# Optimization experiments

Hardware: AMD Instinct MI355X
Metric: run time of the kernel (lower is better)

## Reference

```python
import jax, jax.numpy as jnp
import numpy as np

N_NODES = 50000
N_EDGES = 800000


def gcn_layer(x, edge_index, W, b):
    """PyG-style GCNConv: add self-loops, symmetric deg^-1/2 normalization,
    linear transform, scatter-sum aggregation at target nodes, plus bias."""
    n = x.shape[0]
    loops = jnp.arange(n)
    src = jnp.concatenate([edge_index[0], loops])  # [E+N]
    dst = jnp.concatenate([edge_index[1], loops])  # [E+N]
    deg = jax.ops.segment_sum(jnp.ones(src.shape, dtype=x.dtype), dst, num_segments=n)
    dinv = jnp.where(deg > 0, jax.lax.rsqrt(deg), jnp.zeros((), x.dtype))
    norm = dinv[src] * dinv[dst]               # [E+N]
    h = x @ W                                   # [N, out]
    msg = norm[:, None] * h[src]                # [E+N, out] gather
    out = jax.ops.segment_sum(msg, dst, num_segments=n)  # scatter-add
    return out + b


def setup_inputs() -> dict:
    key = jax.random.key(0)
    ks = jax.random.split(key, 8)
    features = jax.random.normal(ks[0], (N_NODES, 64), dtype=jnp.float32)
    edge_index1 = jax.random.randint(ks[1], (2, N_EDGES), 0, N_NODES)
    edge_index3 = jax.random.randint(ks[2], (2, N_EDGES), 0, N_NODES)
    edge_index9 = jax.random.randint(ks[3], (2, N_EDGES), 0, N_NODES)

    def glorot(k, fi, fo):
        lim = float(np.sqrt(6.0 / (fi + fo)))
        return jax.random.uniform(k, (fi, fo), minval=-lim, maxval=lim, dtype=jnp.float32)

    W1 = glorot(ks[4], 64, 64)
    W2 = glorot(ks[5], 64, 32)
    W3 = glorot(ks[6], 32, 16)
    b1 = jnp.zeros((64,), jnp.float32)
    b2 = jnp.zeros((32,), jnp.float32)
    b3 = jnp.zeros((16,), jnp.float32)
    return dict(features=features, edge_index1=edge_index1, edge_index3=edge_index3,
                edge_index9=edge_index9, W1=W1, b1=b1, W2=W2, b2=b2, W3=W3, b3=b3)


def reference(features, edge_index1, edge_index3, edge_index9, W1, b1, W2, b2, W3, b3):
    x = jax.nn.relu(gcn_layer(features, edge_index1, W1, b1))  # hop 1
    x = jax.nn.relu(gcn_layer(x, edge_index3, W2, b2))         # hop 3
    x = jax.nn.relu(gcn_layer(x, edge_index9, W3, b3))         # hop 9
    return x
```

## Files before the change

kernel.cpp:

```cpp
#include <hip/hip_runtime.h>
#include <hip/hip_fp16.h>


#define NB   256
#define NL   3
#define TB   (NB * NL)
#define CAPE 6400
#define CAPE_E (CAPE + 8)
#define CH   8192
#define P1T  512
#define EPT  (CH / P1T)
#define P2T  512

__device__ __forceinline__ void decode_chunk(int g, int nc1, int nc2,
                                             const int* s1, const int* d1, int E1,
                                             const int* s2, const int* d2, int E2,
                                             const int* s3, const int* d3, int E3,
                                             const int** src, const int** dst, int* E, int* l,
                                             int* gout) {
    if (g < nc1)            { *src = s1; *dst = d1; *E = E1; *l = 0; }
    else if (g < nc1 + nc2) { *src = s2; *dst = d2; *E = E2; *l = 1; g -= nc1; }
    else                    { *src = s3; *dst = d3; *E = E3; *l = 2; g -= nc1 + nc2; }
    *gout = g;
}

__device__ __forceinline__ void fma4(float4& a, float s, const float4& w) {
    a.x += s * w.x; a.y += s * w.y; a.z += s * w.z; a.w += s * w.w;
}
__device__ __forceinline__ void add4(float4& a, const float4& v) {
    a.x += v.x; a.y += v.y; a.z += v.z; a.w += v.w;
}
__device__ __forceinline__ float4 ldh4(const __half* h, size_t idx4) {
    uint2 r = ((const uint2*)h)[idx4];
    __half2 a = *reinterpret_cast<__half2*>(&r.x);
    __half2 b = *reinterpret_cast<__half2*>(&r.y);
    float2 fa = __half22float2(a), fb = __half22float2(b);
    return make_float4(fa.x, fa.y, fb.x, fb.y);
}
__device__ __forceinline__ void sth4(__half* h, size_t idx4, float4 v) {
    __half2 a = __floats2half2_rn(v.x, v.y);
    __half2 b = __floats2half2_rn(v.z, v.w);
    uint2 r;
    r.x = *reinterpret_cast<unsigned*>(&a);
    r.y = *reinterpret_cast<unsigned*>(&b);
    ((uint2*)h)[idx4] = r;
}

__global__ void __launch_bounds__(P1T) k1_phase1_gemm1(
        const int* __restrict__ s1, const int* __restrict__ d1, int E1,
        const int* __restrict__ s2, const int* __restrict__ d2, int E2,
        const int* __restrict__ s3, const int* __restrict__ d3, int E3,
        int nc1, int nc2, int W, int nchunks,
        int* __restrict__ gcur, unsigned int* __restrict__ pairBuf,
        const float* __restrict__ x0, const float* __restrict__ W1g,
        __half* __restrict__ h1) {
    __shared__ __align__(16) char smem[45056];
    const int t = threadIdx.x;
    if (blockIdx.x < (unsigned)nchunks) {
        int* hist = (int*)smem;
        int* eofs = hist + NB;
        int* bo   = eofs + NB;
        int* lcur = bo + NB;
        unsigned* stage = (unsigned*)(smem + 4096);
        unsigned char* stageQ = (unsigned char*)(smem + 36864);
        for (int i = t; i < NB; i += P1T) hist[i] = 0;
        __syncthreads();
        const int* src; const int* dst; int E, l, g;
        decode_chunk(blockIdx.x, nc1, nc2, s1, d1, E1, s2, d2, E2, s3, d3, E3,
                     &src, &dst, &E, &l, &g);
        const int e0 = g * CH;
        const int lbase = l * NB;
        unsigned pv[EPT];
        int bn[EPT];
        if (E - e0 >= CH) {
            const int4* s4 = (const int4*)(src + e0);
            const int4* d4 = (const int4*)(dst + e0);
#pragma unroll
            for (int w = 0; w < EPT / 4; ++w) {
                int4 sv = s4[t + w * P1T];
                int4 dv = d4[t + w * P1T];
                int q, i = w * 4;
                q = dv.x / W; bn[i+0] = q; pv[i+0] = ((unsigned)sv.x << 9) | (unsigned)(dv.x - q * W);
                q = dv.y / W; bn[i+1] = q; pv[i+1] = ((unsigned)sv.y << 9) | (unsigned)(dv.y - q * W);
                q = dv.z / W; bn[i+2] = q; pv[i+2] = ((unsigned)sv.z << 9) | (unsigned)(dv.z - q * W);
                q = dv.w / W; bn[i+3] = q; pv[i+3] = ((unsigned)sv.w << 9) | (unsigned)(dv.w - q * W);
            }
        } else {
#pragma unroll
            for (int i = 0; i < EPT; ++i) {
                int e = e0 + t + i * P1T;
                if (e < E) {
                    int s = src[e], d = dst[e];
                    int q = d / W;
                    bn[i] = q;
                    pv[i] = ((unsigned)s << 9) | (unsigned)(d - q * W);
                } else bn[i] = -1;
            }
        }
#pragma unroll
        for (int i = 0; i < EPT; ++i)
            if (bn[i] >= 0) atomicAdd(&hist[bn[i]], 1);
        __syncthreads();
        if (t < NB) eofs[t] = hist[t];
        __syncthreads();
        for (int off = 1; off < NB; off <<= 1) {
            int add = (t < NB && t >= off) ? eofs[t - off] : 0;
            __syncthreads();
            if (t < NB) eofs[t] += add;
            __syncthreads();
        }
        const int total = eofs[NB - 1];
        int excl = 0;
        if (t < NB) excl = eofs[t] - hist[t];
        __syncthreads();
        if (t < NB) {
            eofs[t] = excl;
            lcur[t] = excl;
            int c = hist[t];
            bo[t] = (lbase + t) * CAPE + (c ? atomicAdd(&gcur[lbase + t], c) : 0);
        }
        __syncthreads();
#pragma unroll
        for (int i = 0; i < EPT; ++i) {
            if (bn[i] >= 0) {
                int r = atomicAdd(&lcur[bn[i]], 1);
                stage[r] = pv[i];
                stageQ[r] = (unsigned char)bn[i];
            }
        }
        __syncthreads();
        for (int i = t; i < total; i += P1T) {
            int q = stageQ[i];
            int k = bo[q] + (i - eofs[q]);
            if (k < (lbase + q + 1) * CAPE) pairBuf[k] = stage[i];
        }
    } else {
        float* Ws = (float*)smem;
        const int bid = blockIdx.x - nchunks;
        for (int i = t; i < 1024; i += P1T)
            ((float4*)Ws)[i] = ((const float4*)W1g)[i];
        __syncthreads();
        const int tc = t % 16;
        const int tr = t / 16;
        const int row0 = bid * 128 + tr * 4;
        const float4* x4 = (const float4*)x0;
        const float4* Ws4 = (const float4*)Ws;
        float4 acc[4];
#pragma unroll
        for (int r = 0; r < 4; ++r) acc[r] = make_float4(0.f, 0.f, 0.f, 0.f);
        int rowc[4];
#pragma unroll
        for (int r = 0; r < 4; ++r) rowc[r] = min(row0 + r, 49999);
        for (int k0 = 0; k0 < 64; k0 += 4) {
            float4 wv0 = Ws4[(k0 + 0) * 16 + tc];
            float4 wv1 = Ws4[(k0 + 1) * 16 + tc];
            float4 wv2 = Ws4[(k0 + 2) * 16 + tc];
            float4 wv3 = Ws4[(k0 + 3) * 16 + tc];
#pragma unroll
            for (int r = 0; r < 4; ++r) {
                float4 xv = x4[(size_t)rowc[r] * 16 + (k0 / 4)];
                fma4(acc[r], xv.x, wv0);
                fma4(acc[r], xv.y, wv1);
                fma4(acc[r], xv.z, wv2);
                fma4(acc[r], xv.w, wv3);
            }
        }
#pragma unroll
        for (int r = 0; r < 4; ++r) {
            int row = row0 + r;
            if (row < 50000) sth4(h1, (size_t)row * 16 + tc, acc[r]);
        }
    }
}

__global__ void __launch_bounds__(P2T) k2_phase2(
        const unsigned int* __restrict__ pairBuf, const int* __restrict__ gcur,
        int n, int W,
        int* __restrict__ row_ptr, int* __restrict__ cnt_g,
        float* __restrict__ dinv, unsigned short* __restrict__ eidx,
        __half* __restrict__ h1) {
    __shared__ __align__(16) char smem[19456];
    int* lcnt  = (int*)smem;
    int* lscan = lcnt + P2T;
    unsigned short* stage = (unsigned short*)(lscan + P2T);
    float* dloc = (float*)(smem + 17408);
    const int bid = blockIdx.x;
    const int l = bid / NB, k = bid % NB;
    const int lo = k * W;
    const int hi = min(n, lo + W);
    const int Wn = hi - lo;
    const int segE = min(gcur[bid], CAPE);
    const size_t base  = (size_t)bid * CAPE;
    const int    baseE = bid * CAPE_E;
    const int t = threadIdx.x;
    lcnt[t] = 0;
    __syncthreads();
    for (int i = t; i < segE; i += P2T)
        atomicAdd(&lcnt[pairBuf[base + i] & 511u], 1);
    __syncthreads();
    const int v = lcnt[t];
    const int vp = (v + 3) & ~3;
    lscan[t] = vp;
    __syncthreads();
    for (int off = 1; off < P2T; off <<= 1) {
        int add = (t >= off) ? lscan[t - off] : 0;
        __syncthreads();
        lscan[t] += add;
        __syncthreads();
    }
    const int pexcl = lscan[t] - vp;
    const int segEp = lscan[P2T - 1];
    if (t < Wn) {
        int node = l * n + lo + t;
        row_ptr[node] = baseE + pexcl;
        cnt_g[node] = v;
        float dv = rsqrtf((float)v + 1.0f);
        dinv[node] = dv;
        dloc[t] = dv;
    }
    __syncthreads();
    lcnt[t] = pexcl;
    __syncthreads();
    const bool lds_ok = (segEp <= CAPE);
    for (int i = t; i < segE; i += P2T) {
        unsigned p = pairBuf[base + i];
        int pos = atomicAdd(&lcnt[p & 511u], 1);
        unsigned short s = (unsigned short)(p >> 9);
        if (lds_ok) stage[pos] = s;
        else if (pos < CAPE_E) eidx[baseE + pos] = s;
    }
    __syncthreads();
    if (lds_ok) {
        const int4* st4 = (const int4*)stage;
        int4* e4 = (int4*)(eidx + baseE);
        int m16 = (segEp + 7) >> 3;
        for (int i = t; i < m16; i += P2T) e4[i] = st4[i];
    }
    if (l == 0) {
        for (int i = t; i < Wn * 16; i += P2T) {
            int r = i >> 4, c = i & 15;
            size_t idx = (size_t)(lo + r) * 16 + c;
            float4 vv = ldh4(h1, idx);
            float s = dloc[r];
            vv.x *= s; vv.y *= s; vv.z *= s; vv.w *= s;
            sth4(h1, idx, vv);
        }
    }
}

__global__ void __launch_bounds__(256) k3_gather1_gemm2(
        const int* __restrict__ row_ptr, const int* __restrict__ cnt,
        const unsigned short* __restrict__ eidx, const float* __restrict__ dinv1,
        const float* __restrict__ dinv2,
        const __half* __restrict__ h1, const float* __restrict__ b1,
        const float* __restrict__ W2g, __half* __restrict__ h2, int n) {
    __shared__ float xs[16 * 68];
    __shared__ float W2s[64 * 32];
    for (int i = threadIdx.x; i < 512; i += 256)
        ((float4*)W2s)[i] = ((const float4*)W2g)[i];
    const int ln = threadIdx.x >> 4;
    const int f4 = threadIdx.x & 15;
    const int node = blockIdx.x * 16 + ln;
    if (node < n) {
        const int beg = row_ptr[node];
        const int m = cnt[node];
        float4 a0 = make_float4(0.f, 0.f, 0.f, 0.f), a1 = a0, a2 = a0, a3 = a0;
        int j = 0;
        for (; j + 8 <= m; j += 8) {
            ushort4 e0 = *(const ushort4*)(eidx + beg + j);
            ushort4 e1 = *(const ushort4*)(eidx + beg + j + 4);
            add4(a0, ldh4(h1, (size_t)e0.x * 16 + f4));
            add4(a1, ldh4(h1, (size_t)e0.y * 16 + f4));
            add4(a2, ldh4(h1, (size_t)e0.z * 16 + f4));
            add4(a3, ldh4(h1, (size_t)e0.w * 16 + f4));
            add4(a0, ldh4(h1, (size_t)e1.x * 16 + f4));
            add4(a1, ldh4(h1, (size_t)e1.y * 16 + f4));
            add4(a2, ldh4(h1, (size_t)e1.z * 16 + f4));
            add4(a3, ldh4(h1, (size_t)e1.w * 16 + f4));
        }
        if (j + 4 <= m) {
            ushort4 e0 = *(const ushort4*)(eidx + beg + j);
            add4(a0, ldh4(h1, (size_t)e0.x * 16 + f4));
            add4(a1, ldh4(h1, (size_t)e0.y * 16 + f4));
            add4(a2, ldh4(h1, (size_t)e0.z * 16 + f4));
            add4(a3, ldh4(h1, (size_t)e0.w * 16 + f4));
            j += 4;
        }
        for (; j < m; ++j)
            add4(a0, ldh4(h1, (size_t)eidx[beg + j] * 16 + f4));
        add4(a0, a1); add4(a2, a3); add4(a0, a2);
        float di = dinv1[node];
        float4 self = ldh4(h1, (size_t)node * 16 + f4);
        float4 bv = ((const float4*)b1)[f4];
        float4 o;
        o.x = di * (a0.x + self.x) + bv.x;
        o.y = di * (a0.y + self.y) + bv.y;
        o.z = di * (a0.z + self.z) + bv.z;
        o.w = di * (a0.w + self.w) + bv.w;
        o.x = o.x > 0.f ? o.x : 0.f;
        o.y = o.y > 0.f ? o.y : 0.f;
        o.z = o.z > 0.f ? o.z : 0.f;
        o.w = o.w > 0.f ? o.w : 0.f;
        *(float4*)&xs[ln * 68 + f4 * 4] = o;
    }
    __syncthreads();
    if (node < n) {
        const int c0 = f4 * 2;
        float s0 = 0.f, s1 = 0.f;
#pragma unroll
        for (int k = 0; k < 64; ++k) {
            float xv = xs[ln * 68 + k];
            s0 += xv * W2s[k * 32 + c0];
            s1 += xv * W2s[k * 32 + c0 + 1];
        }
        float d2 = dinv2[node];
        ((__half2*)h2)[(size_t)node * 16 + f4] = __floats2half2_rn(s0 * d2, s1 * d2);
    }
}

__global__ void __launch_bounds__(256) k4_gather2_gemm3(
        const int* __restrict__ row_ptr2, const int* __restrict__ cnt2,
        const unsigned short* __restrict__ eidx, const float* __restrict__ dinv2,
        const float* __restrict__ dinv3,
        const __half* __restrict__ h2, const float* __restrict__ b2,
        const float* __restrict__ W3g, __half* __restrict__ h3, int n) {
    __shared__ float xs[32 * 36];
    __shared__ float W3s[32 * 16];
    for (int i = threadIdx.x; i < 128; i += 256)
        ((float4*)W3s)[i] = ((const float4*)W3g)[i];
    const int ln = threadIdx.x >> 3;
    const int f4 = threadIdx.x & 7;
    const int node = blockIdx.x * 32 + ln;
    if (node < n) {
        const int beg = row_ptr2[node];
        const int m = cnt2[node];
        float4 a0 = make_float4(0.f, 0.f, 0.f, 0.f), a1 = a0, a2 = a0, a3 = a0;
        int j = 0;
        for (; j + 8 <= m; j += 8) {
            ushort4 e0 = *(const ushort4*)(eidx + beg + j);
            ushort4 e1 = *(const ushort4*)(eidx + beg + j + 4);
            add4(a0, ldh4(h2, (size_t)e0.x * 8 + f4));
            add4(a1, ldh4(h2, (size_t)e0.y * 8 + f4));
            add4(a2, ldh4(h2, (size_t)e0.z * 8 + f4));
            add4(a3, ldh4(h2, (size_t)e0.w * 8 + f4));
            add4(a0, ldh4(h2, (size_t)e1.x * 8 + f4));
            add4(a1, ldh4(h2, (size_t)e1.y * 8 + f4));
            add4(a2, ldh4(h2, (size_t)e1.z * 8 + f4));
            add4(a3, ldh4(h2, (size_t)e1.w * 8 + f4));
        }
        if (j + 4 <= m) {
            ushort4 e0 = *(const ushort4*)(eidx + beg + j);
            add4(a0, ldh4(h2, (size_t)e0.x * 8 + f4));
            add4(a1, ldh4(h2, (size_t)e0.y * 8 + f4));
            add4(a2, ldh4(h2, (size_t)e0.z * 8 + f4));
            add4(a3, ldh4(h2, (size_t)e0.w * 8 + f4));
            j += 4;
        }
        for (; j < m; ++j)
            add4(a0, ldh4(h2, (size_t)eidx[beg + j] * 8 + f4));
        add4(a0, a1); add4(a2, a3); add4(a0, a2);
        float di = dinv2[node];
        float4 self = ldh4(h2, (size_t)node * 8 + f4);
        float4 bv = ((const float4*)b2)[f4];
        float4 o;
        o.x = di * (a0.x + self.x) + bv.x;
        o.y = di * (a0.y + self.y) + bv.y;
        o.z = di * (a0.z + self.z) + bv.z;
        o.w = di * (a0.w + self.w) + bv.w;
        o.x = o.x > 0.f ? o.x : 0.f;
        o.y = o.y > 0.f ? o.y : 0.f;
        o.z = o.z > 0.f ? o.z : 0.f;
        o.w = o.w > 0.f ? o.w : 0.f;
        *(float4*)&xs[ln * 36 + f4 * 4] = o;
    }
    __syncthreads();
    if (node < n) {
        const int c0 = f4 * 2;
        float s0 = 0.f, s1 = 0.f;
#pragma unroll
        for (int k = 0; k < 32; ++k) {
            float xv = xs[ln * 36 + k];
            s0 += xv * W3s[k * 16 + c0];
            s1 += xv * W3s[k * 16 + c0 + 1];
        }
        float d3 = dinv3[node];
        ((__half2*)h3)[(size_t)node * 8 + f4] = __floats2half2_rn(s0 * d3, s1 * d3);
    }
}

__global__ void __launch_bounds__(256) k5_gather3(
        const int* __restrict__ row_ptr3, const int* __restrict__ cnt3,
        const unsigned short* __restrict__ eidx, const float* __restrict__ dinv3,
        const __half* __restrict__ h3, const float* __restrict__ b3,
        float* __restrict__ out, int n) {
    const int ln = threadIdx.x >> 2;
    const int f4 = threadIdx.x & 3;
    const int node = blockIdx.x * 64 + ln;
    if (node >= n) return;
    const int beg = row_ptr3[node];
    const int m = cnt3[node];
    float4 a0 = make_float4(0.f, 0.f, 0.f, 0.f), a1 = a0, a2 = a0, a3 = a0;
    int j = 0;
    for (; j + 8 <= m; j += 8) {
        ushort4 e0 = *(const ushort4*)(eidx + beg + j);
        ushort4 e1 = *(const ushort4*)(eidx + beg + j + 4);
        add4(a0, ldh4(h3, (size_t)e0.x * 4 + f4));
        add4(a1, ldh4(h3, (size_t)e0.y * 4 + f4));
        add4(a2, ldh4(h3, (size_t)e0.z * 4 + f4));
        add4(a3, ldh4(h3, (size_t)e0.w * 4 + f4));
        add4(a0, ldh4(h3, (size_t)e1.x * 4 + f4));
        add4(a1, ldh4(h3, (size_t)e1.y * 4 + f4));
        add4(a2, ldh4(h3, (size_t)e1.z * 4 + f4));
        add4(a3, ldh4(h3, (size_t)e1.w * 4 + f4));
    }
    if (j + 4 <= m) {
        ushort4 e0 = *(const ushort4*)(eidx + beg + j);
        add4(a0, ldh4(h3, (size_t)e0.x * 4 + f4));
        add4(a1, ldh4(h3, (size_t)e0.y * 4 + f4));
        add4(a2, ldh4(h3, (size_t)e0.z * 4 + f4));
        add4(a3, ldh4(h3, (size_t)e0.w * 4 + f4));
        j += 4;
    }
    for (; j < m; ++j)
        add4(a0, ldh4(h3, (size_t)eidx[beg + j] * 4 + f4));
    add4(a0, a1); add4(a2, a3); add4(a0, a2);
    float di = dinv3[node];
    float4 self = ldh4(h3, (size_t)node * 4 + f4);
    float4 bv = ((const float4*)b3)[f4];
    float4 o;
    o.x = di * (a0.x + self.x) + bv.x;
    o.y = di * (a0.y + self.y) + bv.y;
    o.z = di * (a0.z + self.z) + bv.z;
    o.w = di * (a0.w + self.w) + bv.w;
    o.x = o.x > 0.f ? o.x : 0.f;
    o.y = o.y > 0.f ? o.y : 0.f;
    o.z = o.z > 0.f ? o.z : 0.f;
    o.w = o.w > 0.f ? o.w : 0.f;
    ((float4*)out)[(size_t)node * 4 + f4] = o;
}

extern "C" void kernel_launch(void* const* d_in, const int* in_sizes, int n_in,
                              void* d_out, int out_size, void* d_ws, size_t ws_size,
                              hipStream_t stream) {
    const float* x0  = (const float*)d_in[0];
    const int*   ei1 = (const int*)d_in[1];
    const int*   ei3 = (const int*)d_in[2];
    const int*   ei9 = (const int*)d_in[3];
    const float* W1  = (const float*)d_in[4];
    const float* b1  = (const float*)d_in[5];
    const float* W2  = (const float*)d_in[6];
    const float* b2  = (const float*)d_in[7];
    const float* W3  = (const float*)d_in[8];
    const float* b3  = (const float*)d_in[9];

    const int n  = in_sizes[0] / 64;
    const int E1 = in_sizes[1] / 2;
    const int E3 = in_sizes[2] / 2;
    const int E9 = in_sizes[3] / 2;
    const int n3 = 3 * n;
    const int W  = (n + NB - 1) / NB;

    const int nc1 = (E1 + CH - 1) / CH;
    const int nc2 = (E3 + CH - 1) / CH;
    const int nc3 = (E9 + CH - 1) / CH;
    const int nchunks = nc1 + nc2 + nc3;
    const int gemmBlks = (n + 127) / 128;

    int* gcur    = (int*)d_ws;
    unsigned int* pairBuf = (unsigned int*)(gcur + TB);
    unsigned short* eidx = (unsigned short*)(pairBuf + (size_t)TB * CAPE);
    int* row_ptr = (int*)(eidx + (size_t)TB * CAPE_E);
    int* cnt     = row_ptr + n3;
    float* dinv  = (float*)(cnt + n3);
    __half* h1   = (__half*)(dinv + n3);
    __half* h2   = h1 + (size_t)n * 64;
    __half* h3   = h2 + (size_t)n * 32;

    hipMemsetAsync(gcur, 0, TB * sizeof(int), stream);
    k1_phase1_gemm1<<<nchunks + gemmBlks, P1T, 0, stream>>>(
        ei1, ei1 + E1, E1, ei3, ei3 + E3, E3, ei9, ei9 + E9, E9,
        nc1, nc2, W, nchunks, gcur, pairBuf, x0, W1, h1);
    k2_phase2<<<TB, P2T, 0, stream>>>(
        pairBuf, gcur, n, W, row_ptr, cnt, dinv, eidx, h1);
    k3_gather1_gemm2<<<(n + 15) / 16, 256, 0, stream>>>(
        row_ptr, cnt, eidx, dinv, dinv + n, h1, b1, W2, h2, n);
    k4_gather2_gemm3<<<(n + 31) / 32, 256, 0, stream>>>(
        row_ptr + n, cnt + n, eidx, dinv + n, dinv + 2 * n, h2, b2, W3, h3, n);
    k5_gather3<<<(n + 63) / 64, 256, 0, stream>>>(
        row_ptr + 2 * n, cnt + 2 * n, eidx, dinv + 2 * n, h3, b3, (float*)d_out, n);
}
```

Baseline: 162.6 us.

## Sort nodes by in-degree within each bucket to balance gather warps

Phase 2 now runs a 256-element bitonic sort of each bucket's nodes keyed by in-degree and writes a per-layer node permutation. The three gather kernels process nodes in that permuted order, so nodes with similar edge counts share a wavefront and lanes diverge less. The cost is extra syncthreads-heavy sort work in phase 2, an extra indirection load per node, and scattered output and self-feature accesses instead of contiguous ones.

```diff
diff --git a/kernel.cpp b/kernel.cpp
--- a/kernel.cpp
+++ b/kernel.cpp
@@ -178,12 +178,13 @@
         int n, int W,
         int* __restrict__ row_ptr, int* __restrict__ cnt_g,
         float* __restrict__ dinv, unsigned short* __restrict__ eidx,
-        __half* __restrict__ h1) {
-    __shared__ __align__(16) char smem[19456];
+        __half* __restrict__ h1, int* __restrict__ perm) {
+    __shared__ __align__(16) char smem[20480];
     int* lcnt  = (int*)smem;
     int* lscan = lcnt + P2T;
     unsigned short* stage = (unsigned short*)(lscan + P2T);
     float* dloc = (float*)(smem + 17408);
+    unsigned* sortk = (unsigned*)(smem + 19456);
     const int bid = blockIdx.x;
     const int l = bid / NB, k = bid % NB;
     const int lo = k * W;
@@ -246,12 +247,30 @@
             sth4(h1, idx, vv);
         }
     }
+    if (t < 256)
+        sortk[t] = (t < Wn) ? (((unsigned)min(v, 8191) << 9) | (unsigned)t)
+                            : 0xFFFFFFFFu;
+    for (int kk = 2; kk <= 256; kk <<= 1) {
+        for (int j = kk >> 1; j > 0; j >>= 1) {
+            __syncthreads();
+            if (t < 256) {
+                int ixj = t ^ j;
+                if (ixj > t) {
+                    unsigned a = sortk[t], b = sortk[ixj];
+                    bool up = ((t & kk) == 0);
+                    if ((a > b) == up) { sortk[t] = b; sortk[ixj] = a; }
+                }
+            }
+        }
+    }
+    __syncthreads();
+    if (t < Wn) perm[l * n + lo + t] = lo + (int)(sortk[t] & 511u);
 }
 
 __global__ void __launch_bounds__(256) k3_gather1_gemm2(
         const int* __restrict__ row_ptr, const int* __restrict__ cnt,
         const unsigned short* __restrict__ eidx, const float* __restrict__ dinv1,
-        const float* __restrict__ dinv2,
+        const float* __restrict__ dinv2, const int* __restrict__ perm,
         const __half* __restrict__ h1, const float* __restrict__ b1,
         const float* __restrict__ W2g, __half* __restrict__ h2, int n) {
     __shared__ float xs[16 * 68];
@@ -260,8 +279,9 @@
         ((float4*)W2s)[i] = ((const float4*)W2g)[i];
     const int ln = threadIdx.x >> 4;
     const int f4 = threadIdx.x & 15;
-    const int node = blockIdx.x * 16 + ln;
-    if (node < n) {
+    const int gidx = blockIdx.x * 16 + ln;
+    const int node = (gidx < n) ? perm[gidx] : 0;
+    if (gidx < n) {
         const int beg = row_ptr[node];
         const int m = cnt[node];
         float4 a0 = make_float4(0.f, 0.f, 0.f, 0.f), a1 = a0, a2 = a0, a3 = a0;
@@ -304,7 +324,7 @@
         *(float4*)&xs[ln * 68 + f4 * 4] = o;
     }
     __syncthreads();
-    if (node < n) {
+    if (gidx < n) {
         const int c0 = f4 * 2;
         float s0 = 0.f, s1 = 0.f;
 #pragma unroll
@@ -321,7 +341,7 @@
 __global__ void __launch_bounds__(256) k4_gather2_gemm3(
         const int* __restrict__ row_ptr2, const int* __restrict__ cnt2,
         const unsigned short* __restrict__ eidx, const float* __restrict__ dinv2,
-        const float* __restrict__ dinv3,
+        const float* __restrict__ dinv3, const int* __restrict__ perm,
         const __half* __restrict__ h2, const float* __restrict__ b2,
         const float* __restrict__ W3g, __half* __restrict__ h3, int n) {
     __shared__ float xs[32 * 36];
@@ -330,8 +350,9 @@
         ((float4*)W3s)[i] = ((const float4*)W3g)[i];
     const int ln = threadIdx.x >> 3;
     const int f4 = threadIdx.x & 7;
-    const int node = blockIdx.x * 32 + ln;
-    if (node < n) {
+    const int gidx = blockIdx.x * 32 + ln;
+    const int node = (gidx < n) ? perm[gidx] : 0;
+    if (gidx < n) {
         const int beg = row_ptr2[node];
         const int m = cnt2[node];
         float4 a0 = make_float4(0.f, 0.f, 0.f, 0.f), a1 = a0, a2 = a0, a3 = a0;
@@ -374,7 +395,7 @@
         *(float4*)&xs[ln * 36 + f4 * 4] = o;
     }
     __syncthreads();
-    if (node < n) {
+    if (gidx < n) {
         const int c0 = f4 * 2;
         float s0 = 0.f, s1 = 0.f;
 #pragma unroll
@@ -391,12 +412,14 @@
 __global__ void __launch_bounds__(256) k5_gather3(
         const int* __restrict__ row_ptr3, const int* __restrict__ cnt3,
         const unsigned short* __restrict__ eidx, const float* __restrict__ dinv3,
+        const int* __restrict__ perm,
         const __half* __restrict__ h3, const float* __restrict__ b3,
         float* __restrict__ out, int n) {
     const int ln = threadIdx.x >> 2;
     const int f4 = threadIdx.x & 3;
-    const int node = blockIdx.x * 64 + ln;
-    if (node >= n) return;
+    const int gidx = blockIdx.x * 64 + ln;
+    if (gidx >= n) return;
+    const int node = perm[gidx];
     const int beg = row_ptr3[node];
     const int m = cnt3[node];
     float4 a0 = make_float4(0.f, 0.f, 0.f, 0.f), a1 = a0, a2 = a0, a3 = a0;
@@ -472,7 +495,8 @@
     int* row_ptr = (int*)(eidx + (size_t)TB * CAPE_E);
     int* cnt     = row_ptr + n3;
     float* dinv  = (float*)(cnt + n3);
-    __half* h1   = (__half*)(dinv + n3);
+    int* perm    = (int*)(dinv + n3);
+    __half* h1   = (__half*)(perm + n3);
     __half* h2   = h1 + (size_t)n * 64;
     __half* h3   = h2 + (size_t)n * 32;
 
@@ -481,11 +505,11 @@
         ei1, ei1 + E1, E1, ei3, ei3 + E3, E3, ei9, ei9 + E9, E9,
         nc1, nc2, W, nchunks, gcur, pairBuf, x0, W1, h1);
     k2_phase2<<<TB, P2T, 0, stream>>>(
-        pairBuf, gcur, n, W, row_ptr, cnt, dinv, eidx, h1);
+        pairBuf, gcur, n, W, row_ptr, cnt, dinv, eidx, h1, perm);
     k3_gather1_gemm2<<<(n + 15) / 16, 256, 0, stream>>>(
-        row_ptr, cnt, eidx, dinv, dinv + n, h1, b1, W2, h2, n);
+        row_ptr, cnt, eidx, dinv, dinv + n, perm, h1, b1, W2, h2, n);
     k4_gather2_gemm3<<<(n + 31) / 32, 256, 0, stream>>>(
-        row_ptr + n, cnt + n, eidx, dinv + n, dinv + 2 * n, h2, b2, W3, h3, n);
+        row_ptr + n, cnt + n, eidx, dinv + n, dinv + 2 * n, perm + n, h2, b2, W3, h3, n);
     k5_gather3<<<(n + 63) / 64, 256, 0, stream>>>(
-        row_ptr + 2 * n, cnt + 2 * n, eidx, dinv + 2 * n, h3, b3, (float*)d_out, n);
-}
+        row_ptr + 2 * n, cnt + 2 * n, eidx, dinv + 2 * n, perm + 2 * n, h3, b3, (float*)d_out, n);
+}
```

After: 160.3 us. About the same (-1.4%).
